# Optimization experiments

Measured on AMD Instinct MI355X. Metric: run time of the kernel, lower is better.

## Reference

```python
import jax, jax.numpy as jnp
import numpy as np

D = 1024
N_HEAD = 16
D_HEAD = D // N_HEAD


def setup_inputs() -> dict:
    key = jax.random.key(0)
    k1, k2, k3 = jax.random.split(key, 3)
    x = jax.random.normal(k1, (4, 2048, D), dtype=jnp.float32)
    # torch nn.Linear weights: [out_features, in_features]
    W_qkv = jax.random.normal(k2, (3 * D, D), dtype=jnp.float32) * (1.0 / np.sqrt(D))
    W_o = jax.random.normal(k3, (D, D), dtype=jnp.float32) * (1.0 / np.sqrt(D))
    return {"x": x, "W_qkv": W_qkv, "W_o": W_o}


def reference(x, W_qkv, W_o):
    b, s, d = x.shape
    qkv = x @ W_qkv.T                      # [b, s, 3d]
    q, k, v = jnp.split(qkv, 3, axis=-1)
    # [b, s, d] -> [b, h, s, dh]
    def heads(z):
        return z.reshape(b, s, N_HEAD, D_HEAD).transpose(0, 2, 1, 3)
    q, k, v = heads(q), heads(k), heads(v)
    scores = jnp.einsum("bhqd,bhkd->bhqk", q, k) / np.sqrt(D_HEAD).astype(np.float32)
    causal = jnp.tril(jnp.ones((s, s), dtype=bool))  # True = keep
    scores = jnp.where(causal, scores, -jnp.inf)
    attn = jax.nn.softmax(scores, axis=-1)
    out = jnp.einsum("bhqk,bhkd->bhqd", attn, v)     # [b, h, s, dh]
    out = out.transpose(0, 2, 1, 3).reshape(b, s, d)
    return out @ W_o.T
```

## Files before the change

kernel.cpp:

```cpp
#include <hip/hip_runtime.h>


typedef _Float16 f16x8 __attribute__((ext_vector_type(8)));
typedef float floatx4 __attribute__((ext_vector_type(4)));

union U4H8 { uint4 u; f16x8 h; };

__device__ __forceinline__ ushort f32_to_h_bits(float f) {
  _Float16 h = (_Float16)f;
  return __builtin_bit_cast(ushort, h);
}
__device__ __forceinline__ uint pack2h(float a, float b) {
  return (uint)f32_to_h_bits(a) | ((uint)f32_to_h_bits(b) << 16);
}

__device__ __forceinline__ void gld16(const void* g, void* l) {
  __builtin_amdgcn_global_load_lds(
      (const __attribute__((address_space(1))) unsigned char*)g,
      (__attribute__((address_space(3))) unsigned char*)l, 16, 0, 0);
}

__global__ __launch_bounds__(256) void cast_f32_f16(const float* __restrict__ in,
                                                    ushort* __restrict__ out) {
  int i = blockIdx.x * 256 + threadIdx.x;
  float4 v = ((const float4*)in)[i];
  ushort4 o;
  o.x = f32_to_h_bits(v.x);
  o.y = f32_to_h_bits(v.y);
  o.z = f32_to_h_bits(v.z);
  o.w = f32_to_h_bits(v.w);
  ((ushort4*)out)[i] = o;
}

template <int OUT_F16>
__global__ __launch_bounds__(256) void gemm_bt(const ushort* __restrict__ A,
                                               const ushort* __restrict__ B,
                                               void* __restrict__ Cv,
                                               int M, int N, int K) {
  __shared__ ushort As[128 * 32];
  __shared__ ushort Bs[128 * 32];

  const int tid = threadIdx.x;
  const int lane = tid & 63;
  const int wid = tid >> 6;
  const int l15 = lane & 15;
  const int quad = lane >> 4;
  const int m0 = blockIdx.y * 128;
  const int n0 = blockIdx.x * 128;
  const int wm = (wid & 1) * 64;
  const int wn = (wid >> 1) * 64;

  floatx4 acc[4][4];
#pragma unroll
  for (int i = 0; i < 4; i++)
#pragma unroll
    for (int j = 0; j < 4; j++) acc[i][j] = (floatx4){0.f, 0.f, 0.f, 0.f};

  const int srow = tid >> 2;
  const int scol = (tid & 3) * 8;
  const ushort* Ap0 = A + (size_t)(m0 + srow) * K + scol;
  const ushort* Ap1 = A + (size_t)(m0 + 64 + srow) * K + scol;
  const ushort* Bp0 = B + (size_t)(n0 + srow) * K + scol;
  const ushort* Bp1 = B + (size_t)(n0 + 64 + srow) * K + scol;
  ushort* AsW = As + wid * 512;
  ushort* BsW = Bs + wid * 512;

  for (int k0 = 0; k0 < K; k0 += 32) {
    __syncthreads();
    gld16(Ap0 + k0, AsW);
    gld16(Ap1 + k0, AsW + 2048);
    gld16(Bp0 + k0, BsW);
    gld16(Bp1 + k0, BsW + 2048);
    __syncthreads();

    U4H8 af[4], bf[4];
#pragma unroll
    for (int mi = 0; mi < 4; mi++)
      af[mi].u = *(const uint4*)&As[(wm + mi * 16 + l15) * 32 + quad * 8];
#pragma unroll
    for (int ni = 0; ni < 4; ni++)
      bf[ni].u = *(const uint4*)&Bs[(wn + ni * 16 + l15) * 32 + quad * 8];
#pragma unroll
    for (int mi = 0; mi < 4; mi++)
#pragma unroll
      for (int ni = 0; ni < 4; ni++)
        acc[mi][ni] = __builtin_amdgcn_mfma_f32_16x16x32_f16(af[mi].h, bf[ni].h,
                                                             acc[mi][ni], 0, 0, 0);
  }

#pragma unroll
  for (int mi = 0; mi < 4; mi++) {
#pragma unroll
    for (int r = 0; r < 4; r++) {
      size_t row = m0 + wm + mi * 16 + quad * 4 + r;
#pragma unroll
      for (int ni = 0; ni < 4; ni++) {
        size_t col = n0 + wn + ni * 16 + l15;
        float v = acc[mi][ni][r];
        if (OUT_F16)
          ((ushort*)Cv)[row * N + col] = f32_to_h_bits(v);
        else
          ((float*)Cv)[row * N + col] = v;
      }
    }
  }
}

__global__ __launch_bounds__(256) void vtrans(const ushort* __restrict__ qkv,
                                              ushort* __restrict__ vtg) {
  __shared__ ushort T[64 * 66];
  const int tid = threadIdx.x;
  const int kt = blockIdx.x;
  const int bh = blockIdx.y;
  const int b = bh >> 4, h = bh & 15;

  const int r = tid >> 3;
  const int c = (tid & 7) * 8;
  const ushort* src = qkv + (size_t)(b * 2048 + kt * 64) * 3072 + 2048 + h * 64;
  uint4 v0 = *(const uint4*)(src + (size_t)r * 3072 + c);
  uint4 v1 = *(const uint4*)(src + (size_t)(r + 32) * 3072 + c);
  union { uint4 u; ushort s[8]; } a0, a1;
  a0.u = v0; a1.u = v1;
#pragma unroll
  for (int j = 0; j < 8; j++) {
    T[(c + j) * 66 + r] = a0.s[j];
    T[(c + j) * 66 + r + 32] = a1.s[j];
  }
  __syncthreads();

  const int d = tid >> 3;
  const int kc = (tid & 7) * 8;
  ushort* dst = vtg + (size_t)bh * 64 * 2048 + (size_t)kt * 64;
  union { uint u[4]; uint4 u4; } o0, o1;
#pragma unroll
  for (int i = 0; i < 4; i++) {
    o0.u[i] = *(const uint*)&T[d * 66 + kc + 2 * i];
    o1.u[i] = *(const uint*)&T[(d + 32) * 66 + kc + 2 * i];
  }
  *(uint4*)(dst + (size_t)d * 2048 + kc) = o0.u4;
  *(uint4*)(dst + (size_t)(d + 32) * 2048 + kc) = o1.u4;
}

__global__ __launch_bounds__(256, 4) void attn_fused(const ushort* __restrict__ qkv,
                                                     const ushort* __restrict__ vtg,
                                                     ushort* __restrict__ attn_out) {
  __shared__ ushort Ks[2][2][64 * 32];
  __shared__ ushort Vs[2][2][64 * 32];
  __shared__ ushort Ps[4][16 * 40];

  const int tid = threadIdx.x;
  const int lane = tid & 63;
  const int w = tid >> 6;
  const int l15 = lane & 15;
  const int quad = lane >> 4;
  const int bx = blockIdx.x;
  const int bh = blockIdx.y;
  const int b = bh >> 4;
  const int h = bh & 15;
  const int bS = b * 2048;
  const int qtA = bx;
  const int qtB = 31 - bx;
  const int ktmax = qtB;
  int q0s[2];
  q0s[0] = qtA * 64 + w * 16;
  q0s[1] = qtB * 64 + w * 16;

  U4H8 qf[2][2];
#pragma unroll
  for (int s = 0; s < 2; s++) {
    const ushort* qrow = qkv + (size_t)(bS + q0s[s] + l15) * 3072 + h * 64;
#pragma unroll
    for (int kc = 0; kc < 2; kc++) {
      qf[s][kc].u = *(const uint4*)(qrow + kc * 32 + quad * 8);
      qf[s][kc].h = qf[s][kc].h * (_Float16)0.125f;
    }
  }

  floatx4 o[2][4];
#pragma unroll
  for (int s = 0; s < 2; s++)
#pragma unroll
    for (int ni = 0; ni < 4; ni++) o[s][ni] = (floatx4){0.f, 0.f, 0.f, 0.f};
  float m_i[2] = {-1e30f, -1e30f}, l_i[2] = {0.f, 0.f};

  const ushort* kbase = qkv + (size_t)bS * 3072 + 1024 + h * 64;
  const ushort* vbase = vtg + (size_t)bh * 64 * 2048;
  const int srow = lane >> 2;
  const int scc = (lane & 3) * 8;

  auto stage = [&](int kt, int buf) {
    const ushort* kg = kbase + (size_t)(kt * 64 + w * 16 + srow) * 3072 + scc;
    gld16(kg, &Ks[buf][0][w * 512]);
    gld16(kg + 32, &Ks[buf][1][w * 512]);
    const ushort* vg = vbase + (size_t)(w * 16 + srow) * 2048 + kt * 64 + scc;
    gld16(vg, &Vs[buf][0][w * 512]);
    gld16(vg + 32, &Vs[buf][1][w * 512]);
  };

  auto strip_step = [&](int s, bool diag, int kt64, int buf) {
    floatx4 s4[4];
#pragma unroll
    for (int t = 0; t < 4; t++) {
      U4H8 kf0, kf1;
      kf0.u = *(const uint4*)&Ks[buf][0][(t * 16 + l15) * 32 + quad * 8];
      kf1.u = *(const uint4*)&Ks[buf][1][(t * 16 + l15) * 32 + quad * 8];
      floatx4 sa = (floatx4){0.f, 0.f, 0.f, 0.f};
      sa = __builtin_amdgcn_mfma_f32_16x16x32_f16(kf0.h, qf[s][0].h, sa, 0, 0, 0);
      sa = __builtin_amdgcn_mfma_f32_16x16x32_f16(kf1.h, qf[s][1].h, sa, 0, 0, 0);
      s4[t] = sa;
    }
    if (diag) {
      const int q = q0s[s] + l15;
#pragma unroll
      for (int t = 0; t < 4; t++)
#pragma unroll
        for (int r = 0; r < 4; r++) {
          int key = kt64 + t * 16 + quad * 4 + r;
          if (key > q) s4[t][r] = -1e30f;
        }
    }

    float tmax = -1e30f;
#pragma unroll
    for (int t = 0; t < 4; t++)
#pragma unroll
      for (int r = 0; r < 4; r++) tmax = fmaxf(tmax, s4[t][r]);
    tmax = fmaxf(tmax, __shfl_xor(tmax, 16));
    tmax = fmaxf(tmax, __shfl_xor(tmax, 32));
    float mnew = fmaxf(m_i[s], tmax);
    float alpha = __expf(m_i[s] - mnew);
    m_i[s] = mnew;
    float rs = 0.f;
#pragma unroll
    for (int t = 0; t < 4; t++)
#pragma unroll
      for (int r = 0; r < 4; r++) {
        float p = __expf(s4[t][r] - mnew);
        s4[t][r] = p;
        rs += p;
      }
    rs += __shfl_xor(rs, 16);
    rs += __shfl_xor(rs, 32);
    l_i[s] = l_i[s] * alpha + rs;
#pragma unroll
    for (int ni = 0; ni < 4; ni++) o[s][ni] *= alpha;

#pragma unroll
    for (int kc = 0; kc < 2; kc++) {
#pragma unroll
      for (int th = 0; th < 2; th++) {
        const int t = kc * 2 + th;
        *(uint*)&Ps[w][l15 * 40 + th * 16 + quad * 4] = pack2h(s4[t][0], s4[t][1]);
        *(uint*)&Ps[w][l15 * 40 + th * 16 + quad * 4 + 2] = pack2h(s4[t][2], s4[t][3]);
      }
      __asm__ volatile("s_waitcnt lgkmcnt(0)" ::: "memory");
      U4H8 pb;
      pb.u = *(const uint4*)&Ps[w][l15 * 40 + quad * 8];
#pragma unroll
      for (int ni = 0; ni < 4; ni++) {
        U4H8 vf;
        vf.u = *(const uint4*)&Vs[buf][kc][(ni * 16 + l15) * 32 + quad * 8];
        o[s][ni] = __builtin_amdgcn_mfma_f32_16x16x32_f16(vf.h, pb.h, o[s][ni], 0, 0, 0);
      }
    }
  };

  stage(0, 0);
  for (int kt = 0; kt <= ktmax; ++kt) {
    const int buf = kt & 1;
    __syncthreads();
    if (kt < ktmax) stage(kt + 1, buf ^ 1);
    strip_step(1, kt == qtB, kt * 64, buf);
    if (kt <= qtA) strip_step(0, kt == qtA, kt * 64, buf);
  }

#pragma unroll
  for (int s = 0; s < 2; s++) {
    float inv = 1.0f / l_i[s];
    ushort* orow = attn_out + (size_t)(bS + q0s[s] + l15) * 1024 + h * 64;
#pragma unroll
    for (int p = 0; p < 2; p++) {
#pragma unroll
      for (int nh = 0; nh < 2; nh++) {
        const int ni = p * 2 + nh;
        *(uint*)&Ps[w][l15 * 40 + nh * 16 + quad * 4] =
            pack2h(o[s][ni][0] * inv, o[s][ni][1] * inv);
        *(uint*)&Ps[w][l15 * 40 + nh * 16 + quad * 4 + 2] =
            pack2h(o[s][ni][2] * inv, o[s][ni][3] * inv);
      }
      __asm__ volatile("s_waitcnt lgkmcnt(0)" ::: "memory");
      uint4 x = *(const uint4*)&Ps[w][l15 * 40 + quad * 8];
      *(uint4*)(orow + p * 32 + quad * 8) = x;
      __asm__ volatile("s_waitcnt lgkmcnt(0)" ::: "memory");
    }
  }
}

extern "C" void kernel_launch(void* const* d_in, const int* in_sizes, int n_in,
                              void* d_out, int out_size, void* d_ws, size_t ws_size,
                              hipStream_t stream) {
  const float* x = (const float*)d_in[0];
  const float* wqkv = (const float*)d_in[1];
  const float* wo = (const float*)d_in[2];
  float* out = (float*)d_out;

  ushort* xh = (ushort*)d_ws;
  ushort* wqkvh = xh + (size_t)8192 * 1024;
  ushort* woh = wqkvh + (size_t)3072 * 1024;
  ushort* qkvh = woh + (size_t)1024 * 1024;
  ushort* attnh = qkvh + (size_t)8192 * 3072;
  ushort* vtg = attnh + (size_t)8192 * 1024;

  cast_f32_f16<<<8192, 256, 0, stream>>>(x, xh);
  cast_f32_f16<<<3072, 256, 0, stream>>>(wqkv, wqkvh);
  cast_f32_f16<<<1024, 256, 0, stream>>>(wo, woh);

  gemm_bt<1><<<dim3(24, 64), 256, 0, stream>>>(xh, wqkvh, qkvh, 8192, 3072, 1024);
  vtrans<<<dim3(32, 64), 256, 0, stream>>>(qkvh, vtg);
  attn_fused<<<dim3(16, 64), 256, 0, stream>>>(qkvh, vtg, attnh);
  gemm_bt<0><<<dim3(8, 64), 256, 0, stream>>>(attnh, woh, out, 8192, 1024, 1024);
}
```

Baseline: 290.6 us.

## Swizzle LDS tiles and replace P shared-memory staging with ds_bpermute

```diff
diff --git a/kernel.cpp b/kernel.cpp
--- a/kernel.cpp
+++ b/kernel.cpp
@@ -5,6 +5,8 @@
 typedef float floatx4 __attribute__((ext_vector_type(4)));
 
 union U4H8 { uint4 u; f16x8 h; };
+
+__device__ __forceinline__ int swz4(int r) { return (r & 3) ^ ((r >> 2) & 3); }
 
 __device__ __forceinline__ ushort f32_to_h_bits(float f) {
   _Float16 h = (_Float16)f;
@@ -57,13 +59,15 @@
     for (int j = 0; j < 4; j++) acc[i][j] = (floatx4){0.f, 0.f, 0.f, 0.f};
 
   const int srow = tid >> 2;
-  const int scol = (tid & 3) * 8;
+  const int scol = (((tid & 3) ^ swz4(srow & 15)) * 8);
   const ushort* Ap0 = A + (size_t)(m0 + srow) * K + scol;
   const ushort* Ap1 = A + (size_t)(m0 + 64 + srow) * K + scol;
   const ushort* Bp0 = B + (size_t)(n0 + srow) * K + scol;
   const ushort* Bp1 = B + (size_t)(n0 + 64 + srow) * K + scol;
   ushort* AsW = As + wid * 512;
   ushort* BsW = Bs + wid * 512;
+
+  const int rsw = (quad ^ swz4(l15)) * 8;
 
   for (int k0 = 0; k0 < K; k0 += 32) {
     __syncthreads();
@@ -76,10 +80,10 @@
     U4H8 af[4], bf[4];
 #pragma unroll
     for (int mi = 0; mi < 4; mi++)
-      af[mi].u = *(const uint4*)&As[(wm + mi * 16 + l15) * 32 + quad * 8];
+      af[mi].u = *(const uint4*)&As[(wm + mi * 16 + l15) * 32 + rsw];
 #pragma unroll
     for (int ni = 0; ni < 4; ni++)
-      bf[ni].u = *(const uint4*)&Bs[(wn + ni * 16 + l15) * 32 + quad * 8];
+      bf[ni].u = *(const uint4*)&Bs[(wn + ni * 16 + l15) * 32 + rsw];
 #pragma unroll
     for (int mi = 0; mi < 4; mi++)
 #pragma unroll
@@ -146,7 +150,6 @@
                                                      ushort* __restrict__ attn_out) {
   __shared__ ushort Ks[2][2][64 * 32];
   __shared__ ushort Vs[2][2][64 * 32];
-  __shared__ ushort Ps[4][16 * 40];
 
   const int tid = threadIdx.x;
   const int lane = tid & 63;
@@ -165,6 +168,10 @@
   q0s[0] = qtA * 64 + w * 16;
   q0s[1] = qtB * 64 + w * 16;
 
+  const int bpa0 = (l15 + 32 * (quad & 1)) * 4;
+  const int bpa1 = bpa0 + 64;
+  const int selhi = quad >> 1;
+
   U4H8 qf[2][2];
 #pragma unroll
   for (int s = 0; s < 2; s++) {
@@ -186,7 +193,8 @@
   const ushort* kbase = qkv + (size_t)bS * 3072 + 1024 + h * 64;
   const ushort* vbase = vtg + (size_t)bh * 64 * 2048;
   const int srow = lane >> 2;
-  const int scc = (lane & 3) * 8;
+  const int scc = ((lane & 3) ^ swz4(srow)) * 8;
+  const int rsw = (quad ^ swz4(l15)) * 8;
 
   auto stage = [&](int kt, int buf) {
     const ushort* kg = kbase + (size_t)(kt * 64 + w * 16 + srow) * 3072 + scc;
@@ -202,8 +210,8 @@
 #pragma unroll
     for (int t = 0; t < 4; t++) {
       U4H8 kf0, kf1;
-      kf0.u = *(const uint4*)&Ks[buf][0][(t * 16 + l15) * 32 + quad * 8];
-      kf1.u = *(const uint4*)&Ks[buf][1][(t * 16 + l15) * 32 + quad * 8];
+      kf0.u = *(const uint4*)&Ks[buf][0][(t * 16 + l15) * 32 + rsw];
+      kf1.u = *(const uint4*)&Ks[buf][1][(t * 16 + l15) * 32 + rsw];
       floatx4 sa = (floatx4){0.f, 0.f, 0.f, 0.f};
       sa = __builtin_amdgcn_mfma_f32_16x16x32_f16(kf0.h, qf[s][0].h, sa, 0, 0, 0);
       sa = __builtin_amdgcn_mfma_f32_16x16x32_f16(kf1.h, qf[s][1].h, sa, 0, 0, 0);
@@ -245,21 +253,27 @@
 #pragma unroll
     for (int ni = 0; ni < 4; ni++) o[s][ni] *= alpha;
 
+    uint pk[4][2];
+#pragma unroll
+    for (int t = 0; t < 4; t++) {
+      pk[t][0] = pack2h(s4[t][0], s4[t][1]);
+      pk[t][1] = pack2h(s4[t][2], s4[t][3]);
+    }
+
 #pragma unroll
     for (int kc = 0; kc < 2; kc++) {
-#pragma unroll
-      for (int th = 0; th < 2; th++) {
-        const int t = kc * 2 + th;
-        *(uint*)&Ps[w][l15 * 40 + th * 16 + quad * 4] = pack2h(s4[t][0], s4[t][1]);
-        *(uint*)&Ps[w][l15 * 40 + th * 16 + quad * 4 + 2] = pack2h(s4[t][2], s4[t][3]);
-      }
-      __asm__ volatile("s_waitcnt lgkmcnt(0)" ::: "memory");
       U4H8 pb;
-      pb.u = *(const uint4*)&Ps[w][l15 * 40 + quad * 8];
+#pragma unroll
+      for (int i = 0; i < 4; i++) {
+        int addr = (i >> 1) ? bpa1 : bpa0;
+        int lo = __builtin_amdgcn_ds_bpermute(addr, (int)pk[kc * 2][i & 1]);
+        int hi = __builtin_amdgcn_ds_bpermute(addr, (int)pk[kc * 2 + 1][i & 1]);
+        ((uint*)&pb.u)[i] = (uint)(selhi ? hi : lo);
+      }
 #pragma unroll
       for (int ni = 0; ni < 4; ni++) {
         U4H8 vf;
-        vf.u = *(const uint4*)&Vs[buf][kc][(ni * 16 + l15) * 32 + quad * 8];
+        vf.u = *(const uint4*)&Vs[buf][kc][(ni * 16 + l15) * 32 + rsw];
         o[s][ni] = __builtin_amdgcn_mfma_f32_16x16x32_f16(vf.h, pb.h, o[s][ni], 0, 0, 0);
       }
     }
@@ -277,21 +291,24 @@
 #pragma unroll
   for (int s = 0; s < 2; s++) {
     float inv = 1.0f / l_i[s];
+    uint pko[4][2];
+#pragma unroll
+    for (int ni = 0; ni < 4; ni++) {
+      pko[ni][0] = pack2h(o[s][ni][0] * inv, o[s][ni][1] * inv);
+      pko[ni][1] = pack2h(o[s][ni][2] * inv, o[s][ni][3] * inv);
+    }
     ushort* orow = attn_out + (size_t)(bS + q0s[s] + l15) * 1024 + h * 64;
 #pragma unroll
     for (int p = 0; p < 2; p++) {
-#pragma unroll
-      for (int nh = 0; nh < 2; nh++) {
-        const int ni = p * 2 + nh;
-        *(uint*)&Ps[w][l15 * 40 + nh * 16 + quad * 4] =
-            pack2h(o[s][ni][0] * inv, o[s][ni][1] * inv);
-        *(uint*)&Ps[w][l15 * 40 + nh * 16 + quad * 4 + 2] =
-            pack2h(o[s][ni][2] * inv, o[s][ni][3] * inv);
-      }
-      __asm__ volatile("s_waitcnt lgkmcnt(0)" ::: "memory");
-      uint4 x = *(const uint4*)&Ps[w][l15 * 40 + quad * 8];
+      uint4 x;
+#pragma unroll
+      for (int i = 0; i < 4; i++) {
+        int addr = (i >> 1) ? bpa1 : bpa0;
+        int lo = __builtin_amdgcn_ds_bpermute(addr, (int)pko[p * 2][i & 1]);
+        int hi = __builtin_amdgcn_ds_bpermute(addr, (int)pko[p * 2 + 1][i & 1]);
+        ((uint*)&x)[i] = (uint)(selhi ? hi : lo);
+      }
       *(uint4*)(orow + p * 32 + quad * 8) = x;
-      __asm__ volatile("s_waitcnt lgkmcnt(0)" ::: "memory");
     }
   }
 }
```

Measured after the change: 313.2 us. +7.8%, slower.
